# Optimization experiments

Measured on AMD Instinct MI355X. Metric: run time of the kernel, lower is better.

Reference implementation:

```python
import jax, jax.numpy as jnp
import numpy as np

B = 8       # complexes in batch
C = 32      # CDR residues per antibody
G = 2048    # antigen nodes per complex
D = 128     # encoded_dims
N_AB = B * C
N_AG = B * G
N = N_AB + N_AG
SLOPE = 0.2
EPS_BN = 1e-5


def _build_edges():
    # block-sparse bipartite edges (cdr_b x ag_b), symmetrized, + self loops
    srcs, dsts = [], []
    for b in range(B):
        ab = np.arange(b * C, (b + 1) * C)
        ag = np.arange(N_AB + b * G, N_AB + (b + 1) * G)
        g1, g2 = np.meshgrid(ab, ag, indexing='ij')
        srcs.append(g1.ravel()); dsts.append(g2.ravel())
    s = np.concatenate(srcs); d = np.concatenate(dsts)
    loops = np.arange(N)
    src = np.concatenate([s, d, loops]).astype(np.int32)
    dst = np.concatenate([d, s, loops]).astype(np.int32)
    return src, dst


def setup_inputs() -> dict:
    key = jax.random.key(0)
    ks = jax.random.split(key, 16)
    sc = 1.0 / np.sqrt(D)
    edge_src, edge_dst = _build_edges()
    return {
        'selected_ab': jax.random.normal(ks[0], (N_AB, D), jnp.float32),
        'x_ag': jax.random.normal(ks[1], (N_AG, D), jnp.float32),
        'W1': jax.random.normal(ks[2], (D, D), jnp.float32) * sc,
        'a_src1': jax.random.normal(ks[3], (D,), jnp.float32) * sc,
        'a_dst1': jax.random.normal(ks[4], (D,), jnp.float32) * sc,
        'b1': jnp.zeros((D,), jnp.float32),
        'W2': jax.random.normal(ks[5], (D, D), jnp.float32) * sc,
        'a_src2': jax.random.normal(ks[6], (D,), jnp.float32) * sc,
        'a_dst2': jax.random.normal(ks[7], (D,), jnp.float32) * sc,
        'b2': jnp.zeros((D,), jnp.float32),
        'bn_ab_g': jnp.ones((2 * D,), jnp.float32),
        'bn_ab_b': jnp.zeros((2 * D,), jnp.float32),
        'bn_ag_g': jnp.ones((2 * D,), jnp.float32),
        'bn_ag_b': jnp.zeros((2 * D,), jnp.float32),
        'fc_w': jax.random.normal(ks[8], (2 * D, 1), jnp.float32) * sc,
        'fc_b': jnp.zeros((1,), jnp.float32),
        'agfc_w': jax.random.normal(ks[9], (2 * D, 1), jnp.float32) * sc,
        'agfc_b': jnp.zeros((1,), jnp.float32),
        'edge_src': jnp.asarray(edge_src),
        'edge_dst': jnp.asarray(edge_dst),
    }


def _gat(x, W, a_s, a_d, b, src, dst):
    # PyG GATConv, heads=1, eval mode (dropout off)
    h = x @ W                                  # [N, D]
    al_s = h @ a_s                             # [N]
    al_d = h @ a_d                             # [N]
    e = jax.nn.leaky_relu(al_s[src] + al_d[dst], SLOPE)   # [E]
    m = jax.ops.segment_max(e, dst, num_segments=N)
    e = jnp.exp(e - m[dst])
    z = jax.ops.segment_sum(e, dst, num_segments=N)
    alpha = e / (z[dst] + 1e-16)
    out = jax.ops.segment_sum(h[src] * alpha[:, None], dst, num_segments=N)
    return out + b


def _bn(x, g, b):
    # training-mode batch stats (biased variance), like torch BatchNorm1d
    m = x.mean(0)
    v = ((x - m) ** 2).mean(0)
    return (x - m) / jnp.sqrt(v + EPS_BN) * g + b


def reference(selected_ab, x_ag, W1, a_src1, a_dst1, b1, W2, a_src2, a_dst2, b2,
              bn_ab_g, bn_ab_b, bn_ag_g, bn_ag_b, fc_w, fc_b, agfc_w, agfc_b,
              edge_src, edge_dst):
    x = jnp.concatenate([selected_ab, x_ag], axis=0)          # [N, D]
    x = jax.nn.relu(_gat(x, W1, a_src1, a_dst1, b1, edge_src, edge_dst))
    x = _gat(x, W2, a_src2, a_dst2, b2, edge_src, edge_dst)
    x_ab = jnp.concatenate([x[:N_AB], selected_ab], axis=1)   # [N_ab, 2D]
    x_ab = jax.nn.relu(_bn(x_ab, bn_ab_g, bn_ab_b))
    x_ab = (x_ab @ fc_w + fc_b).ravel()
    x_ag_o = jnp.concatenate([x[N_AB:], x_ag], axis=1)        # [N_ag, 2D]
    x_ag_o = jax.nn.relu(_bn(x_ag_o, bn_ag_g, bn_ag_b))
    x_ag_o = (x_ag_o @ agfc_w + agfc_b).ravel()
    return (x_ab, x_ag_o)
```

## Files before the change

kernel.cpp:

```cpp
#include <hip/hip_runtime.h>


#define N_AB 256
#define N_AG 16384
#define N_ALL 16640
#define G_AG 2048
#define SLOPE 0.2f
#define MSHIFT 20.0f

typedef __attribute__((ext_vector_type(4))) float f32x4;
typedef __attribute__((ext_vector_type(8))) __bf16 bf16x8;
typedef __attribute__((ext_vector_type(8))) unsigned short u16x8;
typedef unsigned short ushort_t;

__device__ __forceinline__ float bf2f(ushort_t u) {
  union { unsigned int i; float f; } v; v.i = ((unsigned int)u) << 16; return v.f;
}
__device__ __forceinline__ ushort_t f2bf(float f) {
  union { float fv; unsigned int i; } v; v.fv = f;
  unsigned int x = v.i;
  return (ushort_t)((x + 0x7fffu + ((x >> 16) & 1u)) >> 16);
}
__device__ __forceinline__ float lrelu(float x) { return x >= 0.f ? x : SLOPE * x; }
__device__ __forceinline__ float expw(float e) {
  return __expf(fminf(e, 60.f) - MSHIFT);
}
__device__ __forceinline__ float ldf(const void* p, size_t i, int f) {
  return f ? ((const float*)p)[i] : bf2f(((const ushort_t*)p)[i]);
}
__device__ __forceinline__ void ld8f(const void* p, size_t i, int f, float* o) {
  if (f) {
    const f32x4* q = (const f32x4*)((const float*)p + i);
    f32x4 a = q[0], b = q[1];
#pragma unroll
    for (int j = 0; j < 4; ++j) { o[j] = a[j]; o[j + 4] = b[j]; }
  } else {
    u16x8 v = *(const u16x8*)((const ushort_t*)p + i);
#pragma unroll
    for (int j = 0; j < 8; ++j) o[j] = bf2f(v[j]);
  }
}

__global__ __launch_bounds__(256) void k_pre(
    const void* __restrict__ W1, const void* __restrict__ W2,
    const void* __restrict__ as1, const void* __restrict__ ad1,
    const void* __restrict__ as2, const void* __restrict__ ad2,
    const void* __restrict__ sel_ab,
    ushort_t* __restrict__ W1t, ushort_t* __restrict__ W2t,
    float* __restrict__ va, float* __restrict__ bnsumAG,
    float* __restrict__ accf, float* __restrict__ accz,
    float* __restrict__ selpart, float* __restrict__ selpartq,
    int* __restrict__ flagp) {
  __shared__ float ls[2][128], lq[2][128];
  int t = threadIdx.x, lane = t & 63, wid = t >> 6;
  int bx = blockIdx.x;
  const ushort_t* selu = (const ushort_t*)sel_ab;
  int cnt = 0;
#pragma unroll
  for (int i = 0; i < 8; ++i) {
    unsigned e = (selu[lane * 8 + i] >> 7) & 0xFF;
    if (e > 0xC8) cnt++;
  }
  int f = (__popcll(__ballot(cnt > 0)) >= 3) ? 1 : 0;
  if (bx == 0 && t == 0) flagp[0] = f;

  if (bx < 16) {
    const void* W = (bx < 8) ? W1 : W2;
    ushort_t* Wt = (bx < 8) ? W1t : W2t;
    int base = (bx & 7) * 2048 + t * 8;
    float o[8];
    ld8f(W, base, f, o);
#pragma unroll
    for (int j = 0; j < 8; ++j) {
      int idx = base + j;
      Wt[(idx & 127) * 128 + (idx >> 7)] = f2bf(o[j]);
    }
  } else if (bx < 32) {
    int j = bx - 16;
    const void* W   = (j < 8) ? W1 : W2;
    const void* asv = (j < 8) ? as1 : as2;
    const void* adv = (j < 8) ? ad1 : ad2;
    int vbase = (j < 8) ? 0 : 256;
    int basek = (j & 7) * 16 + wid * 4;
    float a_s0 = ldf(asv, lane, f), a_s1 = ldf(asv, lane + 64, f);
    float a_d0 = ldf(adv, lane, f), a_d1 = ldf(adv, lane + 64, f);
#pragma unroll
    for (int i = 0; i < 4; ++i) {
      int k = basek + i;
      float w0 = ldf(W, (size_t)k * 128 + lane, f);
      float w1 = ldf(W, (size_t)k * 128 + lane + 64, f);
      float ps = w0 * a_s0 + w1 * a_s1;
      float pd = w0 * a_d0 + w1 * a_d1;
#pragma unroll
      for (int o = 1; o < 64; o <<= 1) {
        ps += __shfl_xor(ps, o);
        pd += __shfl_xor(pd, o);
      }
      if (lane == 0) { va[vbase + k] = ps; va[vbase + 128 + k] = pd; }
    }
  } else if (bx < 40) {
    int j = bx - 32;
    f32x4* az = (f32x4*)(accf + (size_t)j * 4096);
    f32x4 z4 = (f32x4){0.f, 0.f, 0.f, 0.f};
    for (int i = t; i < 1024; i += 256) az[i] = z4;
    if (j == 0) { bnsumAG[t] = 0.f; bnsumAG[t + 256] = 0.f; accz[t] = 0.f; }
  } else {
    int j = bx - 40;
    int col = t & 127, rh = t >> 7;
    int r0 = j * 32 + rh * 16;
    float s = 0.f, sq = 0.f;
    for (int r = 0; r < 16; ++r) {
      float v = ldf(sel_ab, (size_t)(r0 + r) * 128 + col, f);
      s += v; sq += v * v;
    }
    ls[rh][col] = s; lq[rh][col] = sq;
    __syncthreads();
    if (t < 128) {
      selpart[j * 128 + t] = ls[0][t] + ls[1][t];
      selpartq[j * 128 + t] = lq[0][t] + lq[1][t];
    }
  }
}

__global__ __launch_bounds__(256) void k_gemm(
    const void* __restrict__ xa, int modeA,
    const void* __restrict__ xb, int modeB,
    const int* __restrict__ flagp,
    const ushort_t* __restrict__ Wt, const float* __restrict__ va,
    ushort_t* __restrict__ h, float* __restrict__ als, float* __restrict__ ald,
    float* __restrict__ accf, float* __restrict__ accz,
    const void* __restrict__ biasAb, float* __restrict__ xabf, int do_abfin) {
  __shared__ float zsh[32], wsh[32];
  int t = threadIdx.x, lane = t & 63, wid = t >> 6;
  int bx = blockIdx.x;
  if (do_abfin && bx < 8) {
    int fr = *flagp;
    int b = bx;
    if (t < 32) {
      int grow = b * 32 + t;
      float w = expw(lrelu(als[grow] + ald[grow]));
      zsh[t] = accz[grow] + w;
      wsh[t] = w;
      accz[grow] = 0.f;
    }
    __syncthreads();
#pragma unroll
    for (int i = 0; i < 16; ++i) {
      int e = i * 256 + t;
      int rl = e >> 7, col = e & 127;
      int grow = b * 32 + rl;
      size_t idx = (size_t)grow * 128 + col;
      float hv = bf2f(h[idx]);
      float v = (accf[idx] + wsh[rl] * hv) / (zsh[rl] + 1e-16f) + ldf(biasAb, col, fr);
      accf[idx] = 0.f;
      v = fmaxf(v, 0.f);
      xabf[idx] = v;
    }
    __syncthreads();
  }

  int rw0 = bx * 32 + (wid >> 1) * 16;
  int ch = wid & 1;
  const void* xsrc; int roff, mode;
  if (rw0 < N_AB) { xsrc = xa; roff = rw0; mode = modeA; }
  else            { xsrc = xb; roff = rw0 - N_AB; mode = modeB; }
  int fx = (mode == 2) ? *flagp : mode;
  int mm = lane & 15, q = lane >> 4;
  f32x4 acc[4];
#pragma unroll
  for (int b = 0; b < 4; ++b) acc[b] = (f32x4){0.f, 0.f, 0.f, 0.f};
  float pals = 0.f, pald = 0.f;
#pragma unroll
  for (int s = 0; s < 4; ++s) {
    int koff = s * 32 + q * 8;
    union { u16x8 u; bf16x8 b; } af;
    float o[8];
    ld8f(xsrc, (size_t)(roff + mm) * 128 + koff, fx, o);
#pragma unroll
    for (int j = 0; j < 8; ++j) {
      af.u[j] = f2bf(o[j]);
      pals += o[j] * va[koff + j];
      pald += o[j] * va[128 + koff + j];
    }
#pragma unroll
    for (int nt = 0; nt < 4; ++nt) {
      int colb = ch * 64 + nt * 16;
      bf16x8 bfr = *(const bf16x8*)(Wt + (size_t)(colb + mm) * 128 + koff);
      acc[nt] = __builtin_amdgcn_mfma_f32_16x16x32_bf16(af.b, bfr, acc[nt], 0, 0, 0);
    }
  }
  if (ch == 0) {
    float s1 = pals; s1 += __shfl_xor(s1, 16); s1 += __shfl_xor(s1, 32);
    float d1 = pald; d1 += __shfl_xor(d1, 16); d1 += __shfl_xor(d1, 32);
    if (lane < 16) { als[rw0 + lane] = s1; ald[rw0 + lane] = d1; }
  }
#pragma unroll
  for (int nt = 0; nt < 4; ++nt)
#pragma unroll
    for (int r = 0; r < 4; ++r) {
      int row = rw0 + q * 4 + r;
      int col = ch * 64 + nt * 16 + mm;
      h[(size_t)row * 128 + col] = f2bf(acc[nt][r]);
    }
}

#define ABP_STRIDE 72
#define AG_STRIDE 40
__global__ __launch_bounds__(256) void k_agg(
    const ushort_t* __restrict__ h, const float* __restrict__ als,
    const float* __restrict__ ald, const void* __restrict__ bias,
    const int* __restrict__ flagp, ushort_t* __restrict__ xout,
    float* __restrict__ accf, float* __restrict__ accz,
    const void* __restrict__ x_ag, float* __restrict__ bnsumAG,
    int do_relu, int do_bnsum) {
  __shared__ ushort_t hT[128 * ABP_STRIDE];
  __shared__ float alsS[64];
  __shared__ float colsum[128], colsq[128];
  int bx = blockIdx.x;
  int t = threadIdx.x, lane = t & 63, wid = t >> 6;
  int mm = lane & 15, q = lane >> 4;

  if (bx < 256) {
    int b = bx >> 5, jt = bx & 31;
    int f = *flagp;
    {
      int row = t & 31, c0g = (t >> 5) * 16;
      const ushort_t* src = h + (size_t)(b * 32 + row) * 128 + c0g;
      u16x8 v0 = *(const u16x8*)src;
      u16x8 v1 = *(const u16x8*)(src + 8);
#pragma unroll
      for (int j = 0; j < 8; ++j) {
        hT[(c0g + j) * AG_STRIDE + row] = v0[j];
        hT[(c0g + 8 + j) * AG_STRIDE + row] = v1[j];
      }
      if (t < 32) alsS[t] = als[b * 32 + t];
      if (t < 128) { colsum[t] = 0.f; colsq[t] = 0.f; }
    }
    __syncthreads();
    int jl = jt * 64 + wid * 16;
    int jrow = N_AB + b * G_AG + jl;
    float aldj = ald[jrow + mm];
    float alsj = als[jrow + mm];
    union { u16x8 u; bf16x8 b; } af;
    float zp = 0.f;
#pragma unroll
    for (int j = 0; j < 8; ++j) {
      ushort_t us = f2bf(expw(lrelu(alsS[q * 8 + j] + aldj)));
      af.u[j] = us;
      zp += bf2f(us);
    }
    zp += __shfl_xor(zp, 16);
    zp += __shfl_xor(zp, 32);
    float wself = expw(lrelu(alsj + aldj));
    float z = zp + wself;
#pragma unroll
    for (int nt = 0; nt < 8; ++nt) {
      int col = nt * 16 + mm;
      union { u16x8 u; bf16x8 b; } bfr;
      bfr.b = *(const bf16x8*)(&hT[col * AG_STRIDE + q * 8]);
      f32x4 acc = {0.f, 0.f, 0.f, 0.f};
      acc = __builtin_amdgcn_mfma_f32_16x16x32_bf16(af.b, bfr.b, acc, 0, 0, 0);
      float biasv = ldf(bias, col, f);
      float sl = 0.f, sq = 0.f;
#pragma unroll
      for (int r = 0; r < 4; ++r) {
        int row = q * 4 + r;
        float zr = __shfl(z, row);
        float wsr = __shfl(wself, row);
        float hv = bf2f(h[(size_t)(jrow + row) * 128 + col]);
        float v = (acc[r] + wsr * hv) / (zr + 1e-16f) + biasv;
        sl += v; sq += v * v;
        if (do_relu) v = fmaxf(v, 0.f);
        xout[(size_t)(jrow + row) * 128 + col] = f2bf(v);
      }
      if (do_bnsum) {
        atomicAdd(&colsum[col], sl);
        atomicAdd(&colsq[col], sq);
      }
    }
    if (do_bnsum) {
      __syncthreads();
      if (t < 128) {
        atomicAdd(&bnsumAG[t], colsum[t]);
        atomicAdd(&bnsumAG[256 + t], colsq[t]);
      }
    }
  } else if (bx < 512) {
    int bx2 = bx - 256;
    int b = bx2 >> 5, sg = bx2 & 31;
    int jrow0 = N_AB + b * G_AG + sg * 64;
    {
      int jr = t & 63, cgrp = (t >> 6) * 32;
      const ushort_t* src = h + (size_t)(jrow0 + jr) * 128 + cgrp;
#pragma unroll
      for (int v = 0; v < 4; ++v) {
        u16x8 vv = *(const u16x8*)(src + v * 8);
#pragma unroll
        for (int j = 0; j < 8; ++j)
          hT[(cgrp + v * 8 + j) * ABP_STRIDE + jr] = vv[j];
      }
      if (t < 64) alsS[t] = als[jrow0 + t];
    }
    __syncthreads();
    float aldm[2] = { ald[b * 32 + mm], ald[b * 32 + 16 + mm] };
    f32x4 acc[2][2];
#pragma unroll
    for (int a = 0; a < 2; ++a)
#pragma unroll
      for (int c = 0; c < 2; ++c) acc[a][c] = (f32x4){0.f, 0.f, 0.f, 0.f};
    float zz[2] = {0.f, 0.f};
#pragma unroll
    for (int s = 0; s < 2; ++s) {
      int k0 = s * 32 + q * 8;
      float a8[8];
#pragma unroll
      for (int j = 0; j < 8; ++j) a8[j] = alsS[k0 + j];
      union { u16x8 u; bf16x8 b; } af[2];
#pragma unroll
      for (int mt = 0; mt < 2; ++mt)
#pragma unroll
        for (int j = 0; j < 8; ++j) {
          ushort_t us = f2bf(expw(lrelu(a8[j] + aldm[mt])));
          af[mt].u[j] = us;
          zz[mt] += bf2f(us);
        }
#pragma unroll
      for (int ns = 0; ns < 2; ++ns) {
        int n = wid * 32 + ns * 16 + mm;
        union { u16x8 u; bf16x8 b; } bfr;
        bfr.b = *(const bf16x8*)(&hT[n * ABP_STRIDE + k0]);
        acc[0][ns] = __builtin_amdgcn_mfma_f32_16x16x32_bf16(af[0].b, bfr.b, acc[0][ns], 0, 0, 0);
        acc[1][ns] = __builtin_amdgcn_mfma_f32_16x16x32_bf16(af[1].b, bfr.b, acc[1][ns], 0, 0, 0);
      }
    }
#pragma unroll
    for (int mt = 0; mt < 2; ++mt)
#pragma unroll
      for (int ns = 0; ns < 2; ++ns)
#pragma unroll
        for (int r = 0; r < 4; ++r) {
          int row = b * 32 + mt * 16 + q * 4 + r;
          int col = wid * 32 + ns * 16 + mm;
          atomicAdd(&accf[(size_t)row * 128 + col], acc[mt][ns][r]);
        }
#pragma unroll
    for (int mt = 0; mt < 2; ++mt) {
      float z = zz[mt];
      z += __shfl_xor(z, 16);
      z += __shfl_xor(z, 32);
      if (wid == 0 && lane < 16)
        atomicAdd(&accz[b * 32 + mt * 16 + lane], z);
    }
  } else {
    int j = bx - 512;
    int f = *flagp;
    int col = t & 127, half = t >> 7;
    int r0 = j * 256 + half * 128;
    float s = 0.f, sq = 0.f;
    for (int r = 0; r < 128; ++r) {
      float v = ldf(x_ag, (size_t)(r0 + r) * 128 + col, f);
      s += v; sq += v * v;
    }
    atomicAdd(&bnsumAG[128 + col], s);
    atomicAdd(&bnsumAG[384 + col], sq);
  }
}

__global__ __launch_bounds__(256) void k_abfin(
    const float* __restrict__ accf, const float* __restrict__ accz,
    const ushort_t* __restrict__ h, const float* __restrict__ als,
    const float* __restrict__ ald, const void* __restrict__ bias,
    const int* __restrict__ flagp, float* __restrict__ xabf,
    float* __restrict__ abpart, float* __restrict__ abpartq,
    const float* __restrict__ bnsumAG,
    const void* __restrict__ gag, const void* __restrict__ bag,
    const void* __restrict__ agfcw, float* __restrict__ statsAG) {
  __shared__ float zsh[8], wsh[8];
  __shared__ float cs[2][128], cq[2][128];
  int bx = blockIdx.x, t = threadIdx.x;
  int f = *flagp;
  if (bx == 32) {
    float mean = bnsumAG[t] * (1.f / 16384.f);
    float var = fmaxf(bnsumAG[256 + t] * (1.f / 16384.f) - mean * mean, 0.f);
    float A = ldf(gag, t, f) / sqrtf(var + 1e-5f);
    statsAG[t] = A;
    statsAG[256 + t] = ldf(bag, t, f) - mean * A;
    statsAG[512 + t] = ldf(agfcw, t, f);
    return;
  }
  int b = bx >> 2, q4 = bx & 3;
  if (t < 8) {
    int grow = b * 32 + q4 * 8 + t;
    float w = expw(lrelu(als[grow] + ald[grow]));
    zsh[t] = accz[grow] + w;
    wsh[t] = w;
  }
  __syncthreads();
  float s = 0.f, sq = 0.f;
#pragma unroll
  for (int i = 0; i < 4; ++i) {
    int e = i * 256 + t;
    int rl = e >> 7, col = e & 127;
    int grow = b * 32 + q4 * 8 + rl;
    size_t idx = (size_t)grow * 128 + col;
    float hv = bf2f(h[idx]);
    float v = (accf[idx] + wsh[rl] * hv) / (zsh[rl] + 1e-16f) + ldf(bias, col, f);
    xabf[idx] = v;
    s += v; sq += v * v;
  }
  cs[t >> 7][t & 127] = s;
  cq[t >> 7][t & 127] = sq;
  __syncthreads();
  if (t < 128) {
    abpart[bx * 128 + t] = cs[0][t] + cs[1][t];
    abpartq[bx * 128 + t] = cq[0][t] + cq[1][t];
  }
}

__global__ __launch_bounds__(256) void k_head(
    const float* __restrict__ xfab, const ushort_t* __restrict__ xfag,
    const void* __restrict__ sel_ab, const void* __restrict__ x_ag,
    const float* __restrict__ statsAG,
    const float* __restrict__ selpart, const float* __restrict__ selpartq,
    const float* __restrict__ abpart, const float* __restrict__ abpartq,
    const void* __restrict__ gab, const void* __restrict__ bab,
    const void* __restrict__ fcw,
    const void* __restrict__ fcb, const void* __restrict__ agfcb,
    const int* __restrict__ flagp, void* __restrict__ out) {
  __shared__ float stA[256], stB[256], stW[256];
  int t = threadIdx.x, lane = t & 63, wid = t >> 6;
  int row = blockIdx.x * 4 + wid;
  int f = *flagp;
  int isAb = (blockIdx.x < 64);
  if (isAb) {
    float s = 0.f, sq = 0.f;
    if (t < 128) {
      for (int j = 0; j < 32; ++j) {
        s += abpart[j * 128 + t];
        sq += abpartq[j * 128 + t];
      }
    } else {
      int c = t - 128;
      for (int j = 0; j < 8; ++j) {
        s += selpart[j * 128 + c];
        sq += selpartq[j * 128 + c];
      }
    }
    float mean = s * (1.f / 256.f);
    float var = fmaxf(sq * (1.f / 256.f) - mean * mean, 0.f);
    float A = ldf(gab, t, f) / sqrtf(var + 1e-5f);
    stA[t] = A;
    stB[t] = ldf(bab, t, f) - mean * A;
    stW[t] = ldf(fcw, t, f);
  } else {
    stA[t] = statsAG[t];
    stB[t] = statsAG[256 + t];
    stW[t] = statsAG[512 + t];
  }
  __syncthreads();

  int c0 = lane * 2;
  float v0, v1, v2, v3, bb;
  if (isAb) {
    const float* p = xfab + (size_t)row * 128 + c0;
    v0 = p[0]; v1 = p[1];
    size_t ro = (size_t)row * 128 + c0;
    v2 = ldf(sel_ab, ro, f);
    v3 = ldf(sel_ab, ro + 1, f);
    bb = ldf(fcb, 0, f);
  } else {
    const ushort_t* p = xfag + (size_t)row * 128 + c0;
    v0 = bf2f(p[0]); v1 = bf2f(p[1]);
    size_t ro = (size_t)(row - N_AB) * 128 + c0;
    v2 = ldf(x_ag, ro, f);
    v3 = ldf(x_ag, ro + 1, f);
    bb = ldf(agfcb, 0, f);
  }
  float acc =
      fmaxf(v0 * stA[c0]           + stB[c0],           0.f) * stW[c0]
    + fmaxf(v1 * stA[c0 + 1]       + stB[c0 + 1],       0.f) * stW[c0 + 1]
    + fmaxf(v2 * stA[128 + c0]     + stB[128 + c0],     0.f) * stW[128 + c0]
    + fmaxf(v3 * stA[128 + c0 + 1] + stB[128 + c0 + 1], 0.f) * stW[128 + c0 + 1];
#pragma unroll
  for (int o = 1; o < 64; o <<= 1) acc += __shfl_xor(acc, o);
  if (lane == 0) {
    float r = acc + bb;
    if (f) ((float*)out)[row] = r;
    else   ((ushort_t*)out)[row] = f2bf(r);
  }
}

extern "C" void kernel_launch(void* const* d_in, const int* in_sizes, int n_in,
                              void* d_out, int out_size, void* d_ws, size_t ws_size,
                              hipStream_t stream) {
  (void)in_sizes; (void)n_in; (void)out_size; (void)ws_size;
  const void* sel_ab = d_in[0];
  const void* x_ag   = d_in[1];
  const void* W1     = d_in[2];
  const void* as1    = d_in[3];
  const void* ad1    = d_in[4];
  const void* b1     = d_in[5];
  const void* W2     = d_in[6];
  const void* as2    = d_in[7];
  const void* ad2    = d_in[8];
  const void* b2     = d_in[9];
  const void* gab    = d_in[10];
  const void* bab    = d_in[11];
  const void* gag    = d_in[12];
  const void* bag    = d_in[13];
  const void* fcw    = d_in[14];
  const void* fcb    = d_in[15];
  const void* agfcw  = d_in[16];
  const void* agfcb  = d_in[17];

  ushort_t* h  = (ushort_t*)d_in[18];
  ushort_t* xb = (ushort_t*)d_in[19];

  char* wsp = (char*)d_ws;
  size_t off = 0;
  auto carve = [&](size_t bytes) -> char* {
    char* p = wsp + off; off += (bytes + 255) & ~(size_t)255; return p;
  };
  int* flag      = (int*)carve(64 * 4);
  ushort_t* W1t  = (ushort_t*)carve(16384 * 2);
  ushort_t* W2t  = (ushort_t*)carve(16384 * 2);
  float* va      = (float*)carve(512 * 4);
  float* als     = (float*)carve((size_t)N_ALL * 4);
  float* ald     = (float*)carve((size_t)N_ALL * 4);
  float* bnsumAG = (float*)carve(512 * 4);
  float* statsAG = (float*)carve(768 * 4);
  float* xabf    = (float*)carve((size_t)N_AB * 128 * 4);
  float* accf    = (float*)carve((size_t)N_AB * 128 * 4);
  float* accz    = (float*)carve(256 * 4);
  float* selpart = (float*)carve(8 * 128 * 4);
  float* selpartq= (float*)carve(8 * 128 * 4);
  float* abpart  = (float*)carve(32 * 128 * 4);
  float* abpartq = (float*)carve(32 * 128 * 4);

  k_pre<<<48, 256, 0, stream>>>(W1, W2, as1, ad1, as2, ad2, sel_ab,
                                W1t, W2t, va, bnsumAG, accf, accz,
                                selpart, selpartq, flag);
  k_gemm<<<520, 256, 0, stream>>>(sel_ab, 2, x_ag, 2, flag, W1t, va, h, als, ald,
                                  accf, accz, b1, xabf, 0);
  k_agg<<<512, 256, 0, stream>>>(h, als, ald, b1, flag, xb, accf, accz,
                                 x_ag, bnsumAG, 1, 0);
  k_gemm<<<520, 256, 0, stream>>>(xabf, 1, xb + (size_t)N_AB * 128, 0, flag, W2t, va + 256, h, als, ald,
                                  accf, accz, b1, xabf, 1);
  k_agg<<<576, 256, 0, stream>>>(h, als, ald, b2, flag, xb, accf, accz,
                                 x_ag, bnsumAG, 0, 1);
  k_abfin<<<33, 256, 0, stream>>>(accf, accz, h, als, ald, b2, flag, xabf,
                                  abpart, abpartq, bnsumAG, gag, bag, agfcw,
                                  statsAG);
  k_head<<<4160, 256, 0, stream>>>(xabf, xb, sel_ab, x_ag, statsAG,
                                   selpart, selpartq, abpart, abpartq,
                                   gab, bab, fcw, fcb, agfcb, flag, d_out);
}
```

Measured before the change: 171.5 us.

## Stage self rows in LDS, move x_ag colsums to first GEMM, batch head rows

The raw x_ag column-sum blocks move from the second aggregation kernel into extra blocks of the first GEMM launch, where they can overlap with the compute-bound GEMM. The antigen aggregation path now copies its 64 self rows of h into shared memory with coalesced vector loads instead of doing strided scalar global reads, and replaces the per-element division with a precomputed reciprocal. The head kernel handles 16 rows per block instead of 4, keeping the BN coefficients in registers, so it launches far fewer blocks. The costs are larger LDS use per block, which may lower occupancy, and slight rounding differences from using reciprocals.

```diff
diff --git a/kernel.cpp b/kernel.cpp
--- a/kernel.cpp
+++ b/kernel.cpp
@@ -129,10 +129,28 @@
     const ushort_t* __restrict__ Wt, const float* __restrict__ va,
     ushort_t* __restrict__ h, float* __restrict__ als, float* __restrict__ ald,
     float* __restrict__ accf, float* __restrict__ accz,
-    const void* __restrict__ biasAb, float* __restrict__ xabf, int do_abfin) {
+    const void* __restrict__ biasAb, float* __restrict__ xabf, int do_abfin,
+    const void* __restrict__ xraw, float* __restrict__ bnsumAG, int do_colsum) {
   __shared__ float zsh[32], wsh[32];
   int t = threadIdx.x, lane = t & 63, wid = t >> 6;
   int bx = blockIdx.x;
+
+  if (do_colsum && bx < 64) {
+    int fr = *flagp;
+    int j = bx;
+    int col = t & 127, half = t >> 7;
+    int r0 = j * 256 + half * 128;
+    float s = 0.f, sq = 0.f;
+    for (int r = 0; r < 128; ++r) {
+      float v = ldf(xraw, (size_t)(r0 + r) * 128 + col, fr);
+      s += v; sq += v * v;
+    }
+    atomicAdd(&bnsumAG[128 + col], s);
+    atomicAdd(&bnsumAG[384 + col], sq);
+    return;
+  }
+  int gbx = do_colsum ? bx - 64 : bx;
+
   if (do_abfin && bx < 8) {
     int fr = *flagp;
     int b = bx;
@@ -159,7 +177,7 @@
     __syncthreads();
   }
 
-  int rw0 = bx * 32 + (wid >> 1) * 16;
+  int rw0 = gbx * 32 + (wid >> 1) * 16;
   int ch = wid & 1;
   const void* xsrc; int roff, mode;
   if (rw0 < N_AB) { xsrc = xa; roff = rw0; mode = modeA; }
@@ -206,14 +224,15 @@
 
 #define ABP_STRIDE 72
 #define AG_STRIDE 40
+#define HS_OFF 5120
+#define HS_STRIDE 136
 __global__ __launch_bounds__(256) void k_agg(
     const ushort_t* __restrict__ h, const float* __restrict__ als,
     const float* __restrict__ ald, const void* __restrict__ bias,
     const int* __restrict__ flagp, ushort_t* __restrict__ xout,
     float* __restrict__ accf, float* __restrict__ accz,
-    const void* __restrict__ x_ag, float* __restrict__ bnsumAG,
-    int do_relu, int do_bnsum) {
-  __shared__ ushort_t hT[128 * ABP_STRIDE];
+    float* __restrict__ bnsumAG, int do_relu, int do_bnsum) {
+  __shared__ ushort_t hT[13824];
   __shared__ float alsS[64];
   __shared__ float colsum[128], colsq[128];
   int bx = blockIdx.x;
@@ -223,6 +242,7 @@
   if (bx < 256) {
     int b = bx >> 5, jt = bx & 31;
     int f = *flagp;
+    int jbase = N_AB + b * G_AG + jt * 64;
     {
       int row = t & 31, c0g = (t >> 5) * 16;
       const ushort_t* src = h + (size_t)(b * 32 + row) * 128 + c0g;
@@ -232,6 +252,15 @@
       for (int j = 0; j < 8; ++j) {
         hT[(c0g + j) * AG_STRIDE + row] = v0[j];
         hT[(c0g + 8 + j) * AG_STRIDE + row] = v1[j];
+      }
+      ushort_t* hS = hT + HS_OFF;
+      const ushort_t* hsrc = h + (size_t)jbase * 128;
+#pragma unroll
+      for (int it = 0; it < 4; ++it) {
+        int e = it * 2048 + t * 8;
+        int rr = e >> 7, cb = e & 127;
+        *(u16x8*)&hS[rr * HS_STRIDE + cb] =
+            *(const u16x8*)(hsrc + (size_t)rr * 128 + cb);
       }
       if (t < 32) alsS[t] = als[b * 32 + t];
       if (t < 128) { colsum[t] = 0.f; colsq[t] = 0.f; }
@@ -253,6 +282,16 @@
     zp += __shfl_xor(zp, 32);
     float wself = expw(lrelu(alsj + aldj));
     float z = zp + wself;
+    float zin[4], wz[4];
+#pragma unroll
+    for (int r = 0; r < 4; ++r) {
+      int rowl = q * 4 + r;
+      float zr = __shfl(z, rowl);
+      float wsr = __shfl(wself, rowl);
+      float inv = 1.0f / (zr + 1e-16f);
+      zin[r] = inv; wz[r] = wsr * inv;
+    }
+    const ushort_t* hSr = hT + HS_OFF + (size_t)(wid * 16) * HS_STRIDE;
 #pragma unroll
     for (int nt = 0; nt < 8; ++nt) {
       int col = nt * 16 + mm;
@@ -265,10 +304,8 @@
 #pragma unroll
       for (int r = 0; r < 4; ++r) {
         int row = q * 4 + r;
-        float zr = __shfl(z, row);
-        float wsr = __shfl(wself, row);
-        float hv = bf2f(h[(size_t)(jrow + row) * 128 + col]);
-        float v = (acc[r] + wsr * hv) / (zr + 1e-16f) + biasv;
+        float hv = bf2f(hSr[row * HS_STRIDE + col]);
+        float v = acc[r] * zin[r] + wz[r] * hv + biasv;
         sl += v; sq += v * v;
         if (do_relu) v = fmaxf(v, 0.f);
         xout[(size_t)(jrow + row) * 128 + col] = f2bf(v);
@@ -285,7 +322,7 @@
         atomicAdd(&bnsumAG[256 + t], colsq[t]);
       }
     }
-  } else if (bx < 512) {
+  } else {
     int bx2 = bx - 256;
     int b = bx2 >> 5, sg = bx2 & 31;
     int jrow0 = N_AB + b * G_AG + sg * 64;
@@ -351,18 +388,6 @@
       if (wid == 0 && lane < 16)
         atomicAdd(&accz[b * 32 + mt * 16 + lane], z);
     }
-  } else {
-    int j = bx - 512;
-    int f = *flagp;
-    int col = t & 127, half = t >> 7;
-    int r0 = j * 256 + half * 128;
-    float s = 0.f, sq = 0.f;
-    for (int r = 0; r < 128; ++r) {
-      float v = ldf(x_ag, (size_t)(r0 + r) * 128 + col, f);
-      s += v; sq += v * v;
-    }
-    atomicAdd(&bnsumAG[128 + col], s);
-    atomicAdd(&bnsumAG[384 + col], sq);
   }
 }
 
@@ -429,9 +454,8 @@
     const int* __restrict__ flagp, void* __restrict__ out) {
   __shared__ float stA[256], stB[256], stW[256];
   int t = threadIdx.x, lane = t & 63, wid = t >> 6;
-  int row = blockIdx.x * 4 + wid;
   int f = *flagp;
-  int isAb = (blockIdx.x < 64);
+  int isAb = (blockIdx.x < 16);
   if (isAb) {
     float s = 0.f, sq = 0.f;
     if (t < 128) {
@@ -460,33 +484,44 @@
   __syncthreads();
 
   int c0 = lane * 2;
-  float v0, v1, v2, v3, bb;
-  if (isAb) {
-    const float* p = xfab + (size_t)row * 128 + c0;
-    v0 = p[0]; v1 = p[1];
-    size_t ro = (size_t)row * 128 + c0;
-    v2 = ldf(sel_ab, ro, f);
-    v3 = ldf(sel_ab, ro + 1, f);
-    bb = ldf(fcb, 0, f);
-  } else {
-    const ushort_t* p = xfag + (size_t)row * 128 + c0;
-    v0 = bf2f(p[0]); v1 = bf2f(p[1]);
-    size_t ro = (size_t)(row - N_AB) * 128 + c0;
-    v2 = ldf(x_ag, ro, f);
-    v3 = ldf(x_ag, ro + 1, f);
-    bb = ldf(agfcb, 0, f);
-  }
-  float acc =
-      fmaxf(v0 * stA[c0]           + stB[c0],           0.f) * stW[c0]
-    + fmaxf(v1 * stA[c0 + 1]       + stB[c0 + 1],       0.f) * stW[c0 + 1]
-    + fmaxf(v2 * stA[128 + c0]     + stB[128 + c0],     0.f) * stW[128 + c0]
-    + fmaxf(v3 * stA[128 + c0 + 1] + stB[128 + c0 + 1], 0.f) * stW[128 + c0 + 1];
-#pragma unroll
-  for (int o = 1; o < 64; o <<= 1) acc += __shfl_xor(acc, o);
-  if (lane == 0) {
-    float r = acc + bb;
-    if (f) ((float*)out)[row] = r;
-    else   ((ushort_t*)out)[row] = f2bf(r);
+  float a0 = stA[c0],        a1 = stA[c0 + 1];
+  float a2 = stA[128 + c0],  a3 = stA[128 + c0 + 1];
+  float g0 = stB[c0],        g1 = stB[c0 + 1];
+  float g2 = stB[128 + c0],  g3 = stB[128 + c0 + 1];
+  float w0 = stW[c0],        w1 = stW[c0 + 1];
+  float w2 = stW[128 + c0],  w3 = stW[128 + c0 + 1];
+  int row0 = isAb ? (blockIdx.x * 16 + wid * 4)
+                  : (N_AB + (blockIdx.x - 16) * 16 + wid * 4);
+  float bb = isAb ? ldf(fcb, 0, f) : ldf(agfcb, 0, f);
+#pragma unroll
+  for (int i = 0; i < 4; ++i) {
+    int row = row0 + i;
+    float v0, v1, v2, v3;
+    if (isAb) {
+      const float* p = xfab + (size_t)row * 128 + c0;
+      v0 = p[0]; v1 = p[1];
+      size_t ro = (size_t)row * 128 + c0;
+      v2 = ldf(sel_ab, ro, f);
+      v3 = ldf(sel_ab, ro + 1, f);
+    } else {
+      const ushort_t* p = xfag + (size_t)row * 128 + c0;
+      v0 = bf2f(p[0]); v1 = bf2f(p[1]);
+      size_t ro = (size_t)(row - N_AB) * 128 + c0;
+      v2 = ldf(x_ag, ro, f);
+      v3 = ldf(x_ag, ro + 1, f);
+    }
+    float acc =
+        fmaxf(v0 * a0 + g0, 0.f) * w0
+      + fmaxf(v1 * a1 + g1, 0.f) * w1
+      + fmaxf(v2 * a2 + g2, 0.f) * w2
+      + fmaxf(v3 * a3 + g3, 0.f) * w3;
+#pragma unroll
+    for (int o = 1; o < 64; o <<= 1) acc += __shfl_xor(acc, o);
+    if (lane == 0) {
+      float r = acc + bb;
+      if (f) ((float*)out)[row] = r;
+      else   ((ushort_t*)out)[row] = f2bf(r);
+    }
   }
 }
 
@@ -540,18 +575,18 @@
   k_pre<<<48, 256, 0, stream>>>(W1, W2, as1, ad1, as2, ad2, sel_ab,
                                 W1t, W2t, va, bnsumAG, accf, accz,
                                 selpart, selpartq, flag);
-  k_gemm<<<520, 256, 0, stream>>>(sel_ab, 2, x_ag, 2, flag, W1t, va, h, als, ald,
-                                  accf, accz, b1, xabf, 0);
+  k_gemm<<<584, 256, 0, stream>>>(sel_ab, 2, x_ag, 2, flag, W1t, va, h, als, ald,
+                                  accf, accz, b1, xabf, 0, x_ag, bnsumAG, 1);
   k_agg<<<512, 256, 0, stream>>>(h, als, ald, b1, flag, xb, accf, accz,
-                                 x_ag, bnsumAG, 1, 0);
+                                 bnsumAG, 1, 0);
   k_gemm<<<520, 256, 0, stream>>>(xabf, 1, xb + (size_t)N_AB * 128, 0, flag, W2t, va + 256, h, als, ald,
-                                  accf, accz, b1, xabf, 1);
-  k_agg<<<576, 256, 0, stream>>>(h, als, ald, b2, flag, xb, accf, accz,
-                                 x_ag, bnsumAG, 0, 1);
+                                  accf, accz, b1, xabf, 1, x_ag, bnsumAG, 0);
+  k_agg<<<512, 256, 0, stream>>>(h, als, ald, b2, flag, xb, accf, accz,
+                                 bnsumAG, 0, 1);
   k_abfin<<<33, 256, 0, stream>>>(accf, accz, h, als, ald, b2, flag, xabf,
                                   abpart, abpartq, bnsumAG, gag, bag, agfcw,
                                   statsAG);
-  k_head<<<4160, 256, 0, stream>>>(xabf, xb, sel_ab, x_ag, statsAG,
+  k_head<<<1040, 256, 0, stream>>>(xabf, xb, sel_ab, x_ag, statsAG,
                                    selpart, selpartq, abpart, abpartq,
                                    gab, bab, fcw, fcb, agfcb, flag, d_out);
 }
```

New measurement: 171.7 us. Within noise of the previous version (+0.1%).
